# Kernel tuning notes

Measured on AMD Instinct MI355X. Metric: run time of the kernel, lower is better.

Reference implementation:

```python
import jax, jax.numpy as jnp
import numpy as np

B = 2048      # batch
L = 128       # signal_length
PL = 8        # patch_length (nodes per graph)
PS = 4        # patch_stride
LW = 4        # local_window
P = (L - PL) // PS + 1   # num_patches = 31
H = 128       # gnn/rnn hidden dim
C = 8         # num_classes


def _mean_adj():
    # A[i, j] = 1/deg(i) for 0 < |i-j| <= LW; exact mean aggregation of SAGEConv
    A = np.zeros((PL, PL), np.float32)
    for i in range(PL):
        nb = [j for j in range(PL) if 0 < abs(i - j) <= LW]
        for j in nb:
            A[i, j] = 1.0 / len(nb)
    return jnp.asarray(A)


def setup_inputs() -> dict:
    key = jax.random.key(0)
    ks = jax.random.split(key, 10)
    def n(k, shape, s):
        return jax.random.normal(k, shape, dtype=jnp.float32) * s
    inp = {
        "iq_signal": jax.random.normal(ks[0], (B, 2, L), dtype=jnp.float32),
        # SAGE layer 0 (in=2 -> H): lin_l (neighbor, with bias), lin_r (root, no bias)
        "Wl0": n(ks[1], (H, 2), 0.3), "bl0": jnp.zeros((H,), jnp.float32), "Wr0": n(ks[2], (H, 2), 0.3),
        # SAGE layers 1-2 (H -> H), stacked
        "Wl12": n(ks[3], (2, H, H), 0.08), "bl12": jnp.zeros((2, H), jnp.float32), "Wr12": n(ks[4], (2, H, H), 0.08),
        # LayerNorm params for the 3 GNN layers
        "ln_gamma": jnp.ones((3, H), jnp.float32), "ln_beta": jnp.zeros((3, H), jnp.float32),
        # 2-layer GRU (input=H, hidden=H), PyTorch gate order [r, z, n]
        "gru_w_ih": n(ks[5], (2, 3 * H, H), 0.08), "gru_w_hh": n(ks[6], (2, 3 * H, H), 0.08),
        "gru_b_ih": jnp.zeros((2, 3 * H), jnp.float32), "gru_b_hh": jnp.zeros((2, 3 * H), jnp.float32),
    }
    # ETF matrix: sqrt(C/(C-1)) * Q @ (I - J/C), Q from QR of random [H, C]
    Pm = jax.random.normal(ks[7], (H, C), dtype=jnp.float32)
    Q, _ = jnp.linalg.qr(Pm)
    I = jnp.eye(C, dtype=jnp.float32)
    J = jnp.ones((C, C), jnp.float32)
    inp["etf"] = (np.float32(np.sqrt(C / (C - 1))) * (Q @ (I - J / C))).astype(jnp.float32)
    return inp


def _layernorm(h, g, b):
    mu = h.mean(-1, keepdims=True)
    var = h.var(-1, keepdims=True)
    return (h - mu) / jnp.sqrt(var + 1e-5) * g + b


def _gru_layer(seq, w_ih, w_hh, b_ih, b_hh):
    # seq: [B, T, H]; precompute input gates for all timesteps
    xg = jnp.einsum('bti,gi->btg', seq, w_ih) + b_ih  # [B, T, 3H]
    def step(hprev, xg_t):
        hg = hprev @ w_hh.T + b_hh
        r = jax.nn.sigmoid(xg_t[:, :H] + hg[:, :H])
        z = jax.nn.sigmoid(xg_t[:, H:2 * H] + hg[:, H:2 * H])
        nn_ = jnp.tanh(xg_t[:, 2 * H:] + r * hg[:, 2 * H:])
        hnew = (1.0 - z) * nn_ + z * hprev
        return hnew, hnew
    h0 = jnp.zeros((seq.shape[0], H), seq.dtype)
    _, outs = jax.lax.scan(step, h0, xg.transpose(1, 0, 2))
    return outs.transpose(1, 0, 2)  # [B, T, H]


def reference(iq_signal, Wl0, bl0, Wr0, Wl12, bl12, Wr12, ln_gamma, ln_beta,
              gru_w_ih, gru_w_hh, gru_b_ih, gru_b_hh, etf):
    # --- DTSG: patch extraction -> [B*P, PL, 2] node features ---
    starts = jnp.arange(P) * PS
    idx = starts[:, None] + jnp.arange(PL)[None, :]       # [P, PL]
    x = iq_signal[:, :, idx]                              # [B, 2, P, PL]
    x = x.transpose(0, 2, 3, 1).reshape(B * P, PL, 2)     # [G, 8, 2]

    A = _mean_adj()  # identical graph for every patch; dense mean-aggregation

    def sage(h, Wl, bl, Wr):
        agg = jnp.einsum('ij,gjf->gif', A, h)             # mean neighbor aggregation
        return jnp.einsum('gif,of->gio', agg, Wl) + bl + jnp.einsum('gif,of->gio', h, Wr)

    # PatchGNN (dropout = identity in eval); edge_attr is ignored by PyG SAGEConv
    h = jax.nn.relu(_layernorm(sage(x, Wl0, bl0, Wr0), ln_gamma[0], ln_beta[0]))
    for i in range(2):
        hn = jax.nn.relu(_layernorm(sage(h, Wl12[i], bl12[i], Wr12[i]), ln_gamma[i + 1], ln_beta[i + 1]))
        h = h + hn  # residual (shapes match for layers 1,2)

    patch_features = h.mean(axis=1)                       # global_mean_pool -> [B*P, H]

    # --- TemporalRNN: 2-layer GRU, take last timestep ---
    seq = patch_features.reshape(B, P, H)
    o = _gru_layer(seq, gru_w_ih[0], gru_w_hh[0], gru_b_ih[0], gru_b_hh[0])
    o = _gru_layer(o, gru_w_ih[1], gru_w_hh[1], gru_b_ih[1], gru_b_hh[1])
    g = o[:, -1, :]                                       # [B, H]

    logits_g = g @ etf                                    # [B, C]
    return logits_g, g, patch_features
```

## Files before the change

### kernel.cpp

```cpp
#include <hip/hip_runtime.h>
#include <hip/hip_bf16.h>

typedef __attribute__((ext_vector_type(8))) short bf16x8;
typedef __attribute__((ext_vector_type(4))) float f32x4;

__device__ __forceinline__ unsigned short f2bf(float v) {
    union { __hip_bfloat16 h; unsigned short u; } cv;
    cv.h = __float2bfloat16(v);
    return cv.u;
}
__device__ __forceinline__ float bf2f(unsigned short u) {
    return __uint_as_float(((unsigned int)u) << 16);
}
__device__ __forceinline__ float sigm(float x) { return 1.f / (1.f + __expf(-x)); }
__device__ __forceinline__ float tanh_(float x) { return 2.f / (1.f + __expf(-2.f * x)) - 1.f; }
__device__ __forceinline__ float adjW(int i, int j) {
    const float inv[8] = {1.f/4.f, 1.f/5.f, 1.f/6.f, 1.f/7.f,
                          1.f/7.f, 1.f/6.f, 1.f/5.f, 1.f/4.f};
    int d = i - j; d = d < 0 ? -d : d;
    return (d >= 1 && d <= 4) ? inv[i] : 0.f;
}

__global__ __launch_bounds__(256) void k0_wconv(const float* __restrict__ Wl12,
    const float* __restrict__ Wr12, const float* __restrict__ wih,
    const float* __restrict__ whh, const float* __restrict__ Wl0,
    const float* __restrict__ Wr0, unsigned short* __restrict__ wbf)
{
    int i = blockIdx.x * 256 + threadIdx.x;
    if (i < 262144) {
        float v; int base, j;
        if (i < 32768)        { v = Wl12[i];        base = (i >> 14) * 16384;           j = i & 16383; }
        else if (i < 65536)   { int s = i - 32768;  v = Wr12[s]; base = 32768 + (s >> 14) * 16384; j = s & 16383; }
        else if (i < 163840)  { int s = i - 65536;  v = wih[s];  base = 65536 + (s / 49152) * 49152; j = s % 49152; }
        else                  { int s = i - 163840; v = whh[s];  base = 163840 + (s / 49152) * 49152; j = s % 49152; }
        int col = j >> 7, k = j & 127;
        int perm = ((col >> 4) * 4 + (k >> 5)) * 512 + ((k >> 3) & 3) * 128 + (col & 15) * 8 + (k & 7);
        wbf[base + perm] = f2bf(v);
    } else {
        int e2 = i - 262144;
        int ct  = e2 >> 9;
        int off = e2 & 511;
        int li2 = off >> 7;
        int rem = off & 127;
        int colLow = rem >> 3;
        int kLow = off & 7;
        int k = li2 * 8 + kLow;
        int col = ct * 16 + colLow;
        float v = 0.f;
        if (k < 2)      v = Wl0[col * 2 + k];
        else if (k < 4) v = Wr0[col * 2 + k - 2];
        wbf[i] = f2bf(v);
    }
}

__global__ __launch_bounds__(256, 4) void k1_sage(
    const float* __restrict__ iq,
    const float* __restrict__ bl0,
    const unsigned short* __restrict__ wbf,
    const float* __restrict__ bl12,
    const float* __restrict__ lng, const float* __restrict__ lnb,
    float* __restrict__ pf)
{
    __shared__ unsigned short hT[64 * 128];
    __shared__ float statS[64][4];
    __shared__ float xS[64][2], axS[64][2];

    const int t  = threadIdx.x;
    const int l  = t & 63;
    const int w  = t >> 6;
    const int wr = w >> 1, wc = w & 1;
    const int lc = l & 15, li = l >> 4;
    const int kgrp = li * 8;
    const int half = li & 1;
    const int g0 = blockIdx.x * 8;

    if (t < 128) {
        int r = t >> 1, c = t & 1;
        int gid = g0 + (r >> 3);
        int node = r & 7;
        int b = gid / 31, p = gid - b * 31;
        xS[r][c] = iq[((size_t)b * 2 + c) * 128 + p * 4 + node];
    }
    __syncthreads();
    if (t < 128) {
        int r = t >> 1, c = t & 1;
        int node = r & 7, base = r & ~7;
        float s = 0.f;
        #pragma unroll
        for (int j = 0; j < 8; ++j) s += adjW(node, j) * xS[base + j][c];
        axS[r][c] = s;
    }
    __syncthreads();

    f32x4 acc[2][4];

    auto ln_epi = [&](const float* gptr, const float* btptr, bool resid) {
        float rs[2][4], rq[2][4];
        #pragma unroll
        for (int mt = 0; mt < 2; ++mt) {
            #pragma unroll
            for (int q = 0; q < 4; ++q) { rs[mt][q] = 0.f; rq[mt][q] = 0.f; }
            #pragma unroll
            for (int nt = 0; nt < 4; ++nt)
                #pragma unroll
                for (int q = 0; q < 4; ++q) {
                    float v = acc[mt][nt][q];
                    rs[mt][q] += v; rq[mt][q] += v * v;
                }
            #pragma unroll
            for (int q = 0; q < 4; ++q)
                #pragma unroll
                for (int m = 1; m < 16; m <<= 1) {
                    rs[mt][q] += __shfl_xor(rs[mt][q], m, 64);
                    rq[mt][q] += __shfl_xor(rq[mt][q], m, 64);
                }
        }
        if (lc == 0) {
            #pragma unroll
            for (int mt = 0; mt < 2; ++mt)
                #pragma unroll
                for (int q = 0; q < 4; ++q) {
                    int row = wr * 32 + mt * 16 + li * 4 + q;
                    statS[row][wc * 2]     = rs[mt][q];
                    statS[row][wc * 2 + 1] = rq[mt][q];
                }
        }
        __syncthreads();
        float gam[4], bet[4];
        #pragma unroll
        for (int nt = 0; nt < 4; ++nt) {
            int col = wc * 64 + nt * 16 + lc;
            gam[nt] = gptr[col]; bet[nt] = btptr[col];
        }
        #pragma unroll
        for (int mt = 0; mt < 2; ++mt)
            #pragma unroll
            for (int q = 0; q < 4; ++q) {
                int row = wr * 32 + mt * 16 + li * 4 + q;
                int s8 = (row & 7) << 3;
                float4 st = *(const float4*)&statS[row][0];
                float sum = st.x + st.z, sq = st.y + st.w;
                float mu   = sum * (1.f / 128.f);
                float var  = sq * (1.f / 128.f) - mu * mu;
                float rstd = rsqrtf(var + 1e-5f);
                #pragma unroll
                for (int nt = 0; nt < 4; ++nt) {
                    int col = wc * 64 + nt * 16 + lc;
                    int idx = row * 128 + (col ^ s8);
                    float v = (acc[mt][nt][q] - mu) * rstd * gam[nt] + bet[nt];
                    v = fmaxf(v, 0.f);
                    float hn = resid ? (bf2f(hT[idx]) + v) : v;
                    hT[idx] = f2bf(hn);
                }
            }
        __syncthreads();
    };

    {
        bf16x8 xA[2];
        #pragma unroll
        for (int mt = 0; mt < 2; ++mt) {
            bf16x8 v = (bf16x8){0, 0, 0, 0, 0, 0, 0, 0};
            if (li == 0) {
                int row = wr * 32 + mt * 16 + lc;
                v[0] = (short)f2bf(axS[row][0]); v[1] = (short)f2bf(axS[row][1]);
                v[2] = (short)f2bf(xS[row][0]);  v[3] = (short)f2bf(xS[row][1]);
            }
            xA[mt] = v;
        }
        const unsigned short* w0f = wbf + 262144;
        #pragma unroll
        for (int nt = 0; nt < 4; ++nt) {
            float bv = bl0[wc * 64 + nt * 16 + lc];
            acc[0][nt] = (f32x4){bv, bv, bv, bv};
            acc[1][nt] = (f32x4){bv, bv, bv, bv};
        }
        #pragma unroll
        for (int nt = 0; nt < 4; ++nt) {
            bf16x8 b0 = *(const bf16x8*)&w0f[(wc * 4 + nt) * 512 + l * 8];
            acc[0][nt] = __builtin_amdgcn_mfma_f32_16x16x32_bf16(xA[0], b0, acc[0][nt], 0, 0, 0);
            acc[1][nt] = __builtin_amdgcn_mfma_f32_16x16x32_bf16(xA[1], b0, acc[1][nt], 0, 0, 0);
        }
        ln_epi(lng, lnb, false);
    }

    const int aswz = (lc & 7) << 3;
    #pragma unroll 1
    for (int lay = 0; lay < 2; ++lay) {
        bf16x8 hA[2][4];
        #pragma unroll
        for (int mt = 0; mt < 2; ++mt)
            #pragma unroll
            for (int ks = 0; ks < 4; ++ks) {
                int row = wr * 32 + 16 * mt + lc;
                hA[mt][ks] = *(const bf16x8*)&hT[row * 128 + ((ks * 32 + kgrp) ^ aswz)];
            }

        const unsigned short* wl  = wbf + lay * 16384;
        const unsigned short* wrp = wbf + 32768 + lay * 16384;

        #pragma unroll
        for (int mt = 0; mt < 2; ++mt)
            #pragma unroll
            for (int nt = 0; nt < 4; ++nt) acc[mt][nt] = (f32x4){0.f, 0.f, 0.f, 0.f};

        #pragma unroll
        for (int ks = 0; ks < 4; ++ks) {
            #pragma unroll
            for (int nt = 0; nt < 4; ++nt) {
                bf16x8 b = *(const bf16x8*)&wl[((wc * 4 + nt) * 4 + ks) * 512 + l * 8];
                acc[0][nt] = __builtin_amdgcn_mfma_f32_16x16x32_bf16(hA[0][ks], b, acc[0][nt], 0, 0, 0);
                acc[1][nt] = __builtin_amdgcn_mfma_f32_16x16x32_bf16(hA[1][ks], b, acc[1][nt], 0, 0, 0);
            }
        }

        #pragma unroll
        for (int mt = 0; mt < 2; ++mt)
            #pragma unroll
            for (int nt = 0; nt < 4; ++nt) {
                float own[4], oth[4];
                #pragma unroll
                for (int q = 0; q < 4; ++q) {
                    own[q] = acc[mt][nt][q];
                    oth[q] = __shfl_xor(own[q], 16, 64);
                }
                float yL[4], yH[4];
                #pragma unroll
                for (int q = 0; q < 4; ++q) {
                    yL[q] = half ? oth[q] : own[q];
                    yH[q] = half ? own[q] : oth[q];
                }
                float S = yL[0]+yL[1]+yL[2]+yL[3]+yH[0]+yH[1]+yH[2]+yH[3];
                float o0, o1, o2, o3;
                if (!half) {
                    o0 = (S - yL[0] - yH[1] - yH[2] - yH[3]) * 0.25f;
                    o1 = (S - yL[1] - yH[2] - yH[3]) * 0.2f;
                    o2 = (S - yL[2] - yH[3]) * (1.f/6.f);
                    o3 = (S - yL[3]) * (1.f/7.f);
                } else {
                    o0 = (S - yH[0]) * (1.f/7.f);
                    o1 = (S - yH[1] - yL[0]) * (1.f/6.f);
                    o2 = (S - yH[2] - yL[0] - yL[1]) * 0.2f;
                    o3 = (S - yH[3] - yL[0] - yL[1] - yL[2]) * 0.25f;
                }
                acc[mt][nt][0] = o0; acc[mt][nt][1] = o1;
                acc[mt][nt][2] = o2; acc[mt][nt][3] = o3;
            }

        #pragma unroll
        for (int nt = 0; nt < 4; ++nt) {
            float bv = bl12[lay * 128 + wc * 64 + nt * 16 + lc];
            #pragma unroll
            for (int mt = 0; mt < 2; ++mt)
                #pragma unroll
                for (int q = 0; q < 4; ++q) acc[mt][nt][q] += bv;
        }

        #pragma unroll
        for (int ks = 0; ks < 4; ++ks) {
            #pragma unroll
            for (int nt = 0; nt < 4; ++nt) {
                bf16x8 b = *(const bf16x8*)&wrp[((wc * 4 + nt) * 4 + ks) * 512 + l * 8];
                acc[0][nt] = __builtin_amdgcn_mfma_f32_16x16x32_bf16(hA[0][ks], b, acc[0][nt], 0, 0, 0);
                acc[1][nt] = __builtin_amdgcn_mfma_f32_16x16x32_bf16(hA[1][ks], b, acc[1][nt], 0, 0, 0);
            }
        }

        ln_epi(lng + (lay + 1) * 128, lnb + (lay + 1) * 128, true);
    }

    {
        const int gi = t >> 5, c0 = t & 31;
        #pragma unroll
        for (int k = 0; k < 4; ++k) {
            int c = c0 + 32 * k;
            float s = 0.f;
            #pragma unroll
            for (int j = 0; j < 8; ++j)
                s += bf2f(hT[(gi * 8 + j) * 128 + (c ^ (j << 3))]);
            pf[(size_t)(g0 + gi) * 128 + c] = s * 0.125f;
        }
    }
}

__global__ __launch_bounds__(256) void k2_xg(
    const float* __restrict__ src, const unsigned short* __restrict__ wB,
    const float* __restrict__ bias, unsigned short* __restrict__ out)
{
    const int t = threadIdx.x, w = t >> 6, l = t & 63;
    const int lc = l & 15, li = l >> 4;
    const int m0 = blockIdx.x * 64 + w * 16;

    bf16x8 aA[4];
    #pragma unroll
    for (int ks = 0; ks < 4; ++ks) {
        const float* p = src + (size_t)(m0 + lc) * 128 + ks * 32 + li * 8;
        float4 f0 = *(const float4*)p;
        float4 f1 = *(const float4*)(p + 4);
        bf16x8 v;
        v[0] = (short)f2bf(f0.x); v[1] = (short)f2bf(f0.y);
        v[2] = (short)f2bf(f0.z); v[3] = (short)f2bf(f0.w);
        v[4] = (short)f2bf(f1.x); v[5] = (short)f2bf(f1.y);
        v[6] = (short)f2bf(f1.z); v[7] = (short)f2bf(f1.w);
        aA[ks] = v;
    }
    #pragma unroll 2
    for (int nt = 0; nt < 24; ++nt) {
        float bv = bias[nt * 16 + lc];
        f32x4 acc = (f32x4){bv, bv, bv, bv};
        #pragma unroll
        for (int ks = 0; ks < 4; ++ks) {
            bf16x8 b = *(const bf16x8*)&wB[(size_t)(nt * 4 + ks) * 512 + l * 8];
            acc = __builtin_amdgcn_mfma_f32_16x16x32_bf16(aA[ks], b, acc, 0, 0, 0);
        }
        #pragma unroll
        for (int q = 0; q < 4; ++q) {
            int m = m0 + li * 4 + q;
            out[(size_t)m * 384 + nt * 16 + lc] = f2bf(acc[q]);
        }
    }
}

__global__ __launch_bounds__(512, 2) void k3_gru(
    const unsigned short* __restrict__ xg, const unsigned short* __restrict__ wbf,
    const float* __restrict__ bih, const float* __restrict__ bhh,
    float* __restrict__ gbuf)
{
    __shared__ unsigned short h1S[16][136];
    __shared__ unsigned short h2S[16][136];

    const int t = threadIdx.x, w = t >> 6, l = t & 63;
    const int lc = l & 15, li = l >> 4;
    const int col = w * 16 + lc;
    const int kgrp = li * 8;
    const int b0 = blockIdx.x * 8;
    const bool act = (li < 2);

    for (int i = t; i < 16 * 136; i += 512) {
        ((unsigned short*)h1S)[i] = 0;
        ((unsigned short*)h2S)[i] = 0;
    }

    const unsigned short* wih2 = wbf + 114688;
    const unsigned short* whh1 = wbf + 163840;
    const unsigned short* whh2 = wbf + 212992;
    bf16x8 Wh1[3][4], Wi2[3][4], Wh2[3][4];
    #pragma unroll
    for (int g = 0; g < 3; ++g)
        #pragma unroll
        for (int ks = 0; ks < 4; ++ks) {
            size_t off = (size_t)((g * 8 + w) * 4 + ks) * 512 + l * 8;
            Wh1[g][ks] = *(const bf16x8*)(whh1 + off);
            Wi2[g][ks] = *(const bf16x8*)(wih2 + off);
            Wh2[g][ks] = *(const bf16x8*)(whh2 + off);
        }
    float bh1[3], bi2[3], bh2[3];
    #pragma unroll
    for (int g = 0; g < 3; ++g) {
        bh1[g] = bhh[g * 128 + col];
        bi2[g] = bih[384 + g * 128 + col];
        bh2[g] = bhh[384 + g * 128 + col];
    }

    float h1r[4] = {0.f, 0.f, 0.f, 0.f};
    float h2r[4] = {0.f, 0.f, 0.f, 0.f};
    float x1[3][4];

    if (act) {
        #pragma unroll
        for (int g = 0; g < 3; ++g)
            #pragma unroll
            for (int q = 0; q < 4; ++q)
                x1[g][q] = bf2f(xg[((size_t)(b0 + li * 4 + q) * 31 + 0) * 384 + g * 128 + col]);
    }
    __syncthreads();

    for (int ts = 0; ts < 31; ++ts) {
        bf16x8 aH[4];
        #pragma unroll
        for (int ks = 0; ks < 4; ++ks) aH[ks] = *(const bf16x8*)&h1S[lc][ks * 32 + kgrp];
        f32x4 acc[3];
        #pragma unroll
        for (int g = 0; g < 3; ++g) {
            acc[g] = (f32x4){0.f, 0.f, 0.f, 0.f};
            #pragma unroll
            for (int ks = 0; ks < 4; ++ks)
                acc[g] = __builtin_amdgcn_mfma_f32_16x16x32_bf16(aH[ks], Wh1[g][ks], acc[g], 0, 0, 0);
        }
        float xn[3][4];
        if (act && ts < 30) {
            #pragma unroll
            for (int g = 0; g < 3; ++g)
                #pragma unroll
                for (int q = 0; q < 4; ++q)
                    xn[g][q] = bf2f(xg[((size_t)(b0 + li * 4 + q) * 31 + ts + 1) * 384 + g * 128 + col]);
        }
        if (act) {
            #pragma unroll
            for (int q = 0; q < 4; ++q) {
                float r  = sigm(x1[0][q] + acc[0][q] + bh1[0]);
                float z  = sigm(x1[1][q] + acc[1][q] + bh1[1]);
                float nn = tanh_(x1[2][q] + r * (acc[2][q] + bh1[2]));
                h1r[q] = (1.f - z) * nn + z * h1r[q];
            }
        }
        __syncthreads();
        if (act) {
            #pragma unroll
            for (int q = 0; q < 4; ++q) h1S[li * 4 + q][col] = f2bf(h1r[q]);
        }
        __syncthreads();

        bf16x8 aH1n[4], aH2[4];
        #pragma unroll
        for (int ks = 0; ks < 4; ++ks) {
            aH1n[ks] = *(const bf16x8*)&h1S[lc][ks * 32 + kgrp];
            aH2[ks]  = *(const bf16x8*)&h2S[lc][ks * 32 + kgrp];
        }
        f32x4 ax2[3], ah2[3];
        #pragma unroll
        for (int g = 0; g < 3; ++g) {
            ax2[g] = (f32x4){0.f, 0.f, 0.f, 0.f};
            ah2[g] = (f32x4){0.f, 0.f, 0.f, 0.f};
            #pragma unroll
            for (int ks = 0; ks < 4; ++ks) {
                ax2[g] = __builtin_amdgcn_mfma_f32_16x16x32_bf16(aH1n[ks], Wi2[g][ks], ax2[g], 0, 0, 0);
                ah2[g] = __builtin_amdgcn_mfma_f32_16x16x32_bf16(aH2[ks],  Wh2[g][ks], ah2[g], 0, 0, 0);
            }
        }
        if (act) {
            #pragma unroll
            for (int q = 0; q < 4; ++q) {
                float xr = ax2[0][q] + bi2[0];
                float xz = ax2[1][q] + bi2[1];
                float xn2 = ax2[2][q] + bi2[2];
                float r  = sigm(xr + ah2[0][q] + bh2[0]);
                float z  = sigm(xz + ah2[1][q] + bh2[1]);
                float nn = tanh_(xn2 + r * (ah2[2][q] + bh2[2]));
                h2r[q] = (1.f - z) * nn + z * h2r[q];
            }
        }
        __syncthreads();
        if (act) {
            #pragma unroll
            for (int q = 0; q < 4; ++q) h2S[li * 4 + q][col] = f2bf(h2r[q]);
        }
        __syncthreads();

        #pragma unroll
        for (int g = 0; g < 3; ++g)
            #pragma unroll
            for (int q = 0; q < 4; ++q) x1[g][q] = xn[g][q];
    }

    if (act) {
        #pragma unroll
        for (int q = 0; q < 4; ++q)
            gbuf[(size_t)(b0 + li * 4 + q) * 128 + col] = h2r[q];
    }
}

__global__ __launch_bounds__(256) void k4_logits(
    const float* __restrict__ g, const float* __restrict__ etf, float* __restrict__ logits)
{
    const int idx = blockIdx.x * 256 + threadIdx.x;
    const int b = idx >> 3, c = idx & 7;
    float s = 0.f;
    #pragma unroll 8
    for (int f = 0; f < 128; ++f) s += g[(size_t)b * 128 + f] * etf[f * 8 + c];
    logits[idx] = s;
}

extern "C" void kernel_launch(void* const* d_in, const int* in_sizes, int n_in,
                              void* d_out, int out_size, void* d_ws, size_t ws_size,
                              hipStream_t stream) {
    const float* iq   = (const float*)d_in[0];
    const float* Wl0  = (const float*)d_in[1];
    const float* bl0  = (const float*)d_in[2];
    const float* Wr0  = (const float*)d_in[3];
    const float* Wl12 = (const float*)d_in[4];
    const float* bl12 = (const float*)d_in[5];
    const float* Wr12 = (const float*)d_in[6];
    const float* lng  = (const float*)d_in[7];
    const float* lnb  = (const float*)d_in[8];
    const float* wih  = (const float*)d_in[9];
    const float* whh  = (const float*)d_in[10];
    const float* bih  = (const float*)d_in[11];
    const float* bhh  = (const float*)d_in[12];
    const float* etf  = (const float*)d_in[13];

    float* out    = (float*)d_out;
    float* logits = out;
    float* gbuf   = out + 16384;
    float* pf     = out + 16384 + 262144;

    unsigned short* wbf = (unsigned short*)d_ws;
    unsigned short* xg  = wbf + 266240;

    k0_wconv<<<1040, 256, 0, stream>>>(Wl12, Wr12, wih, whh, Wl0, Wr0, wbf);
    k1_sage<<<7936, 256, 0, stream>>>(iq, bl0, wbf, bl12, lng, lnb, pf);
    k2_xg<<<992, 256, 0, stream>>>(pf, wbf + 65536, bih, xg);
    k3_gru<<<256, 512, 0, stream>>>(xg, wbf, bih, bhh, gbuf);
    k4_logits<<<64, 256, 0, stream>>>(gbuf, etf, logits);
}
```

Baseline: 336.0 us.

## Keep residual state in fp32 registers and pool patches from registers

The SAGE kernel now keeps the per-thread hidden state in registers (hPrev) at full fp32 precision. Residual adds read from those registers instead of re-reading bf16 values from LDS. The final layer skips its LDS write and barrier, and the mean pool is computed from registers with a cross-lane shuffle. This raises register use, so the launch-bounds occupancy hint drops from 4 to 3 blocks per CU, which may cut the latency hiding available.

```diff
diff --git a/kernel.cpp b/kernel.cpp
--- a/kernel.cpp
+++ b/kernel.cpp
@@ -53,7 +53,7 @@
     }
 }
 
-__global__ __launch_bounds__(256, 4) void k1_sage(
+__global__ __launch_bounds__(256, 3) void k1_sage(
     const float* __restrict__ iq,
     const float* __restrict__ bl0,
     const unsigned short* __restrict__ wbf,
@@ -93,8 +93,9 @@
     __syncthreads();
 
     f32x4 acc[2][4];
-
-    auto ln_epi = [&](const float* gptr, const float* btptr, bool resid) {
+    f32x4 hPrev[2][4];
+
+    auto ln_epi = [&](const float* gptr, const float* btptr, bool resid, bool writeHT) {
         float rs[2][4], rq[2][4];
         #pragma unroll
         for (int mt = 0; mt < 2; ++mt) {
@@ -146,14 +147,14 @@
                 #pragma unroll
                 for (int nt = 0; nt < 4; ++nt) {
                     int col = wc * 64 + nt * 16 + lc;
-                    int idx = row * 128 + (col ^ s8);
                     float v = (acc[mt][nt][q] - mu) * rstd * gam[nt] + bet[nt];
                     v = fmaxf(v, 0.f);
-                    float hn = resid ? (bf2f(hT[idx]) + v) : v;
-                    hT[idx] = f2bf(hn);
-                }
-            }
-        __syncthreads();
+                    float hn = resid ? (hPrev[mt][nt][q] + v) : v;
+                    hPrev[mt][nt][q] = hn;
+                    if (writeHT) hT[row * 128 + (col ^ s8)] = f2bf(hn);
+                }
+            }
+        if (writeHT) __syncthreads();
     };
 
     {
@@ -181,7 +182,7 @@
             acc[0][nt] = __builtin_amdgcn_mfma_f32_16x16x32_bf16(xA[0], b0, acc[0][nt], 0, 0, 0);
             acc[1][nt] = __builtin_amdgcn_mfma_f32_16x16x32_bf16(xA[1], b0, acc[1][nt], 0, 0, 0);
         }
-        ln_epi(lng, lnb, false);
+        ln_epi(lng, lnb, false, true);
     }
 
     const int aswz = (lc & 7) << 3;
@@ -266,19 +267,20 @@
             }
         }
 
-        ln_epi(lng + (lay + 1) * 128, lnb + (lay + 1) * 128, true);
-    }
-
-    {
-        const int gi = t >> 5, c0 = t & 31;
-        #pragma unroll
-        for (int k = 0; k < 4; ++k) {
-            int c = c0 + 32 * k;
-            float s = 0.f;
-            #pragma unroll
-            for (int j = 0; j < 8; ++j)
-                s += bf2f(hT[(gi * 8 + j) * 128 + (c ^ (j << 3))]);
-            pf[(size_t)(g0 + gi) * 128 + c] = s * 0.125f;
+        ln_epi(lng + (lay + 1) * 128, lnb + (lay + 1) * 128, true, lay == 0);
+    }
+
+    #pragma unroll
+    for (int mt = 0; mt < 2; ++mt) {
+        #pragma unroll
+        for (int nt = 0; nt < 4; ++nt) {
+            float s = hPrev[mt][nt][0] + hPrev[mt][nt][1]
+                    + hPrev[mt][nt][2] + hPrev[mt][nt][3];
+            s += __shfl_xor(s, 16, 64);
+            if ((li & 1) == 0) {
+                int gi = wr * 4 + mt * 2 + (li >> 1);
+                pf[(size_t)(g0 + gi) * 128 + wc * 64 + nt * 16 + lc] = s * 0.125f;
+            }
         }
     }
 }
```

Result: slower. 367.1 us (+9.3%).
